# Kernel tuning notes

Measured on AMD Instinct MI355X. Metric: run time of the kernel, lower is better.

Reference implementation:

```python
import jax, jax.numpy as jnp
import numpy as np

EPS = 1e-18
MARGIN = 0.2  # hp.margin (cancels: positive/positive == 1)
BIAS = 1.0    # hp.bias


def setup_inputs() -> dict:
    key = jax.random.key(0)
    k1, k2, k3, k4 = jax.random.split(key, 4)
    B, T, D = 32, 256, 256  # T == D required by the broadcast in Ecos_sim
    return {
        "pre_VF": jax.random.normal(k1, (B, T, D), dtype=jnp.float32),
        "pre_AF": jax.random.normal(k2, (B, T, D), dtype=jnp.float32),
        "back_VF": jax.random.normal(k3, (B, T, D), dtype=jnp.float32),
        "back_AF": jax.random.normal(k4, (B, T, D), dtype=jnp.float32),
    }


def _direction_loss(V, A):
    """For each anchor i: log(1 + sum_{j != i} exp(sim(V_i, A_j))).

    sim(V_i, A_j)[t, s] = (V_i @ A_j.T)[t, s] / (||V_i||_F * colnorm(A_j)[s])
    (faithful to Ecos_sim: scalar Frobenius norm for V, per-column norm for A,
    broadcast along the last axis; positive/positive == 1 exactly, so the
    positive term and margin cancel.)
    """
    B = V.shape[0]
    # upper[i,j,t,s] = <V[i,t,:], A[j,s,:]>
    upper = jnp.einsum("itd,jsd->ijts", V, A)
    v_norm = jnp.sqrt(jnp.sum(V ** 2, axis=(1, 2)) + EPS)      # [B]
    a_norm = jnp.sqrt(jnp.sum(A ** 2, axis=1) + EPS)           # [B, D]
    sim = upper / (v_norm[:, None, None, None] * a_norm[None, :, None, :])
    e_sim = jnp.exp(sim)                                        # [B,B,T,T]
    idx = jnp.arange(B)
    down = e_sim.sum(axis=1) - e_sim[idx, idx]                  # exclude j == i
    rows = jnp.log(1.0 + down)                                  # [B,T,T]
    return rows.reshape(-1, rows.shape[-1])                     # cat along dim 0


def reference(pre_VF, pre_AF, back_VF, back_AF):
    sim_back_V = _direction_loss(back_VF, back_AF)
    sim_back_A = _direction_loss(back_AF, back_VF)
    return -(1.0 / BIAS) * (sim_back_V + sim_back_A)
```

## Files before the change

kernel.cpp:

```cpp
#include <hip/hip_runtime.h>
#include <cstdint>

#define R_TOT 8192
#define KD    256
#define SLOT  ((size_t)R_TOT * KD)
#define IVN_OFF  0
#define ICN_OFF  256
#define CSQ_OFF  (ICN_OFF + 65536)
#define MATS_OFF (CSQ_OFF + 524288)

typedef float f32x4 __attribute__((ext_vector_type(4)));
typedef int   i32x4 __attribute__((ext_vector_type(4)));
typedef int   i32x8 __attribute__((ext_vector_type(8)));

__device__ __forceinline__ void glds16(const void* g, void* l){
  __builtin_amdgcn_global_load_lds((const __attribute__((address_space(1))) uint32_t*)g,
                                   (__attribute__((address_space(3))) uint32_t*)l, 16, 0, 0);
}

__global__ void cast_ns_k(const float* __restrict__ V, const float* __restrict__ A,
                          unsigned char* __restrict__ mats, float* __restrict__ csq){
  const int tc = blockIdx.x, j = blockIdx.y, ten = blockIdx.z;
  const int tid = threadIdx.x;
  const int g    = tid & 31;
  const int tsub = tid >> 5;
  const int c    = g >> 1;
  const int half = g & 1;
  const float* X = (ten ? A : V) + (size_t)j * 65536;
  unsigned char* M = mats + (size_t)ten * SLOT + (size_t)j * 65536;
  float cs[8];
  #pragma unroll
  for (int e = 0; e < 8; ++e) cs[e] = 0.f;
  #pragma unroll
  for (int tt = 0; tt < 4; ++tt){
    const int t = tc * 32 + tt * 8 + tsub;
    const float4 p0 = *(const float4*)(X + t * 256 + g * 8);
    const float4 p1 = *(const float4*)(X + t * 256 + g * 8 + 4);
    cs[0] += p0.x * p0.x; cs[1] += p0.y * p0.y; cs[2] += p0.z * p0.z; cs[3] += p0.w * p0.w;
    cs[4] += p1.x * p1.x; cs[5] += p1.y * p1.y; cs[6] += p1.z * p1.z; cs[7] += p1.w * p1.w;
    int d0 = __builtin_amdgcn_cvt_pk_fp8_f32(p0.x, p0.y, 0, false);
    d0     = __builtin_amdgcn_cvt_pk_fp8_f32(p0.z, p0.w, d0, true);
    int d1 = __builtin_amdgcn_cvt_pk_fp8_f32(p1.x, p1.y, 0, false);
    d1     = __builtin_amdgcn_cvt_pk_fp8_f32(p1.z, p1.w, d1, true);
    int2 o; o.x = d0; o.y = d1;
    *(int2*)(M + (size_t)t * 256 + (((c ^ (t & 15)) << 4) | (half << 3))) = o;
  }
  __shared__ float red[8][256];
  #pragma unroll
  for (int e = 0; e < 8; ++e) red[tsub][g * 8 + e] = cs[e];
  __syncthreads();
  float s = 0.f;
  #pragma unroll
  for (int gg = 0; gg < 8; ++gg) s += red[gg][tid];
  csq[(size_t)((tc * 2 + ten) * 32 + j) * 256 + tid] = s;
}

__global__ void nreduce_k(const float* __restrict__ csq, float* __restrict__ ivn,
                          float* __restrict__ icn){
  const int j = blockIdx.x, ten = blockIdx.y, s = threadIdx.x;
  float c = 0.f;
  #pragma unroll
  for (int tc = 0; tc < 8; ++tc)
    c += csq[(size_t)((tc * 2 + ten) * 32 + j) * 256 + s];
  icn[ten * 8192 + j * 256 + s] = rsqrtf(c + 1e-18f);
  __shared__ float red[256];
  red[s] = c; __syncthreads();
  for (int off = 128; off > 0; off >>= 1){
    if (s < off) red[s] += red[s + off];
    __syncthreads();
  }
  if (s == 0) ivn[ten * 32 + j] = rsqrtf(red[0] + 1e-18f);
}

__global__ __launch_bounds__(256, 4) void gemm_both_k(const unsigned char* __restrict__ mats,
                                                      const float* __restrict__ ivn,
                                                      const float* __restrict__ icn,
                                                      float* __restrict__ out){
  __shared__ __align__(16) char smem[40960];
  const int tid  = threadIdx.x;
  const int lane = tid & 63;
  const int w    = tid >> 6;
  const int dir  = w >> 1;
  const int wn   = (w & 1) * 16;
  const int lm   = lane & 15;
  const int kh   = lane >> 4;
  const int s0   = blockIdx.x * 32;
  const int rb   = blockIdx.y;
  const int r0   = rb * 64;
  const int ib   = rb >> 2;

  const unsigned char* rowmat = mats + (size_t)dir * SLOT;
  const unsigned char* colmat = mats + (size_t)(1 - dir) * SLOT;
  const float sivn = ivn[dir * 32 + ib] * 1.44269504088896340736f;

  float* cscw = (float*)(smem + 32768) + w * 512;
  {
    const float* ibase = icn + (size_t)(1 - dir) * 8192 + s0 + wn;
    #pragma unroll
    for (int jx = 0; jx < 8; ++jx){
      const int j = kh * 8 + jx;
      cscw[j * 16 + lm] = sivn * ibase[j * 256 + lm];
    }
  }

  i32x8 afr[4][2];
  #pragma unroll
  for (int mi = 0; mi < 4; ++mi){
    const unsigned char* rp = rowmat + (size_t)(r0 + mi * 16 + lm) * 256;
    #pragma unroll
    for (int t = 0; t < 2; ++t){
      i32x4 lo = *(const i32x4*)(rp + ((((t << 3) | (kh << 1) | 0) ^ lm) << 4));
      i32x4 hi = *(const i32x4*)(rp + ((((t << 3) | (kh << 1) | 1) ^ lm) << 4));
      afr[mi][t] = i32x8{lo.x, lo.y, lo.z, lo.w, hi.x, hi.y, hi.z, hi.w};
    }
  }
  #pragma unroll
  for (int mi = 0; mi < 4; ++mi)
    #pragma unroll
    for (int t = 0; t < 2; ++t)
      asm volatile("" : "+v"(afr[mi][t]));

  char* wbase = smem + w * 8192;
  int ad[2][2];
  #pragma unroll
  for (int t = 0; t < 2; ++t)
    #pragma unroll
    for (int u = 0; u < 2; ++u)
      ad[t][u] = lm * 256 + ((((t << 3) | (kh << 1) | u) ^ lm) << 4);
  const int lo16 = lane * 16;

  f32x4 acc[4];
  #pragma unroll
  for (int mi = 0; mi < 4; ++mi)
    acc[mi] = f32x4{0.f, 0.f, 0.f, 0.f};

  {
    const int j0 = (ib == 0) ? 1 : 0;
    const unsigned char* src = colmat + ((size_t)j0 * 256 + s0 + wn) * 256;
    #pragma unroll
    for (int c = 0; c < 4; ++c)
      glds16(src + c * 1024 + lo16, wbase + c * 1024 + lo16);
  }
  asm volatile("s_waitcnt vmcnt(0) lgkmcnt(0)" ::: "memory");

  for (int jj = 0; jj < 31; ++jj){
    const int j = jj + (jj >= ib ? 1 : 0);

    if (jj < 30){
      const int jn = (jj + 1) + ((jj + 1) >= ib ? 1 : 0);
      const unsigned char* src = colmat + ((size_t)jn * 256 + s0 + wn) * 256;
      char* dst = wbase + (((jj + 1) & 1) << 12);
      #pragma unroll
      for (int c = 0; c < 4; ++c)
        glds16(src + c * 1024 + lo16, dst + c * 1024 + lo16);
      asm volatile("s_waitcnt vmcnt(4)" ::: "memory");
    } else {
      asm volatile("s_waitcnt vmcnt(0)" ::: "memory");
    }

    const char* rbuf = wbase + ((jj & 1) << 12);
    i32x4 lo0 = *(const i32x4*)(rbuf + ad[0][0]);
    i32x4 hi0 = *(const i32x4*)(rbuf + ad[0][1]);
    i32x4 lo1 = *(const i32x4*)(rbuf + ad[1][0]);
    i32x4 hi1 = *(const i32x4*)(rbuf + ad[1][1]);
    const float csc = cscw[j * 16 + lm];

    i32x8 b[2];
    b[0] = i32x8{lo0.x, lo0.y, lo0.z, lo0.w, hi0.x, hi0.y, hi0.z, hi0.w};
    b[1] = i32x8{lo1.x, lo1.y, lo1.z, lo1.w, hi1.x, hi1.y, hi1.z, hi1.w};

    f32x4 S[4];
    #pragma unroll
    for (int mi = 0; mi < 4; ++mi)
      S[mi] = f32x4{0.f, 0.f, 0.f, 0.f};
    #pragma unroll
    for (int t = 0; t < 2; ++t){
      S[0] = __builtin_amdgcn_mfma_scale_f32_16x16x128_f8f6f4(afr[0][t], b[t], S[0], 0, 0, 0, 127, 0, 127);
      S[1] = __builtin_amdgcn_mfma_scale_f32_16x16x128_f8f6f4(afr[1][t], b[t], S[1], 0, 0, 0, 127, 0, 127);
      S[2] = __builtin_amdgcn_mfma_scale_f32_16x16x128_f8f6f4(afr[2][t], b[t], S[2], 0, 0, 0, 127, 0, 127);
      S[3] = __builtin_amdgcn_mfma_scale_f32_16x16x128_f8f6f4(afr[3][t], b[t], S[3], 0, 0, 0, 127, 0, 127);
    }
    #pragma unroll
    for (int mi = 0; mi < 4; ++mi)
      #pragma unroll
      for (int r = 0; r < 4; ++r)
        acc[mi][r] += __builtin_amdgcn_exp2f(S[mi][r] * csc);
  }

  __syncthreads();
  float* ebuf = (float*)smem;
  #pragma unroll
  for (int mi = 0; mi < 4; ++mi){
    const int n = wn + lm;
    #pragma unroll
    for (int r = 0; r < 4; ++r){
      const int m = mi * 16 + (kh << 2) + r;
      ebuf[(dir * 64 + m) * 36 + n] = __logf(1.f + acc[mi][r]);
    }
  }
  __syncthreads();
  #pragma unroll
  for (int p = 0; p < 2; ++p){
    const int i   = tid + p * 256;
    const int row = i >> 3;
    const int c4  = i & 7;
    const f32x4 e0 = *(const f32x4*)(&ebuf[row * 36 + c4 * 4]);
    const f32x4 e1 = *(const f32x4*)(&ebuf[(64 + row) * 36 + c4 * 4]);
    f32x4 o;
    #pragma unroll
    for (int e = 0; e < 4; ++e) o[e] = -(e0[e] + e1[e]);
    *(f32x4*)(&out[(size_t)(r0 + row) * 256 + s0 + c4 * 4]) = o;
  }
}

extern "C" void kernel_launch(void* const* d_in, const int* in_sizes, int n_in,
                              void* d_out, int out_size, void* d_ws, size_t ws_size,
                              hipStream_t stream){
  const float* V = (const float*)d_in[2];
  const float* A = (const float*)d_in[3];
  float* out = (float*)d_out;
  float* ivn = (float*)((char*)d_ws + IVN_OFF);
  float* icn = (float*)((char*)d_ws + ICN_OFF);
  float* csq = (float*)((char*)d_ws + CSQ_OFF);
  unsigned char* mats = (unsigned char*)((char*)d_ws + MATS_OFF);

  cast_ns_k<<<dim3(8, 32, 2), 256, 0, stream>>>(V, A, mats, csq);
  nreduce_k<<<dim3(32, 2), 256, 0, stream>>>(csq, ivn, icn);
  gemm_both_k<<<dim3(8, 128), 256, 0, stream>>>(mats, ivn, icn, out);
}
```

Before: 118.5 us.

## Software-pipeline MFMA and exp stages with ping-pong registers in GEMM loop

The column-tile loop is restructured into a two-stage software pipeline. The MFMAs for tile x are issued while the exp2/accumulate of tile x-1 runs, using ping-pong B fragments and score registers, with sched_barrier and s_setprio to control issue order. The first global-to-LDS prefetch now starts before the A fragments are loaded. Launch bounds drop from 4 to 2 blocks per CU, which frees registers for the doubled state but may lower occupancy from the four blocks per CU that LDS allows.

```diff
diff --git a/kernel.cpp b/kernel.cpp
--- a/kernel.cpp
+++ b/kernel.cpp
@@ -72,7 +72,7 @@
   if (s == 0) ivn[ten * 32 + j] = rsqrtf(red[0] + 1e-18f);
 }
 
-__global__ __launch_bounds__(256, 4) void gemm_both_k(const unsigned char* __restrict__ mats,
+__global__ __launch_bounds__(256, 2) void gemm_both_k(const unsigned char* __restrict__ mats,
                                                       const float* __restrict__ ivn,
                                                       const float* __restrict__ icn,
                                                       float* __restrict__ out){
@@ -93,7 +93,22 @@
   const unsigned char* colmat = mats + (size_t)(1 - dir) * SLOT;
   const float sivn = ivn[dir * 32 + ib] * 1.44269504088896340736f;
 
+  char* wbase = smem + w * 8192;
   float* cscw = (float*)(smem + 32768) + w * 512;
+  const int lo16 = lane * 16;
+  const unsigned char* colbase = colmat + (size_t)(s0 + wn) * 256;
+
+  auto issue = [&](int x){
+    const int j = x + (x >= ib ? 1 : 0);
+    const unsigned char* src = colbase + (size_t)j * 65536;
+    char* dst = wbase + ((x & 1) << 12);
+    #pragma unroll
+    for (int c = 0; c < 4; ++c)
+      glds16(src + c * 1024 + lo16, dst + c * 1024 + lo16);
+  };
+
+  issue(0);
+
   {
     const float* ibase = icn + (size_t)(1 - dir) * 8192 + s0 + wn;
     #pragma unroll
@@ -120,72 +135,91 @@
     for (int t = 0; t < 2; ++t)
       asm volatile("" : "+v"(afr[mi][t]));
 
-  char* wbase = smem + w * 8192;
   int ad[2][2];
   #pragma unroll
   for (int t = 0; t < 2; ++t)
     #pragma unroll
     for (int u = 0; u < 2; ++u)
       ad[t][u] = lm * 256 + ((((t << 3) | (kh << 1) | u) ^ lm) << 4);
-  const int lo16 = lane * 16;
 
   f32x4 acc[4];
   #pragma unroll
   for (int mi = 0; mi < 4; ++mi)
     acc[mi] = f32x4{0.f, 0.f, 0.f, 0.f};
-
-  {
-    const int j0 = (ib == 0) ? 1 : 0;
-    const unsigned char* src = colmat + ((size_t)j0 * 256 + s0 + wn) * 256;
-    #pragma unroll
-    for (int c = 0; c < 4; ++c)
-      glds16(src + c * 1024 + lo16, wbase + c * 1024 + lo16);
-  }
+  const f32x4 fz = {0.f, 0.f, 0.f, 0.f};
+
+  i32x8 bA[2], bB[2];
+  f32x4 SA[4], SB[4];
+  float cscA, cscB;
+
+#define DSREAD(BX, CX, x_) do{                                                  \
+    const char* rbuf_ = wbase + (((x_) & 1) << 12);                             \
+    i32x4 lo0_ = *(const i32x4*)(rbuf_ + ad[0][0]);                             \
+    i32x4 hi0_ = *(const i32x4*)(rbuf_ + ad[0][1]);                             \
+    i32x4 lo1_ = *(const i32x4*)(rbuf_ + ad[1][0]);                             \
+    i32x4 hi1_ = *(const i32x4*)(rbuf_ + ad[1][1]);                             \
+    BX[0] = i32x8{lo0_.x, lo0_.y, lo0_.z, lo0_.w, hi0_.x, hi0_.y, hi0_.z, hi0_.w}; \
+    BX[1] = i32x8{lo1_.x, lo1_.y, lo1_.z, lo1_.w, hi1_.x, hi1_.y, hi1_.z, hi1_.w}; \
+    const int j_ = (x_) + ((x_) >= ib ? 1 : 0);                                 \
+    CX = cscw[j_ * 16 + lm];                                                    \
+  }while(0)
+
+#define MFMA8(SX, BX) do{                                                       \
+    SX[0] = __builtin_amdgcn_mfma_scale_f32_16x16x128_f8f6f4(afr[0][0], BX[0], fz,    0, 0, 0, 127, 0, 127); \
+    SX[1] = __builtin_amdgcn_mfma_scale_f32_16x16x128_f8f6f4(afr[1][0], BX[0], fz,    0, 0, 0, 127, 0, 127); \
+    SX[2] = __builtin_amdgcn_mfma_scale_f32_16x16x128_f8f6f4(afr[2][0], BX[0], fz,    0, 0, 0, 127, 0, 127); \
+    SX[3] = __builtin_amdgcn_mfma_scale_f32_16x16x128_f8f6f4(afr[3][0], BX[0], fz,    0, 0, 0, 127, 0, 127); \
+    SX[0] = __builtin_amdgcn_mfma_scale_f32_16x16x128_f8f6f4(afr[0][1], BX[1], SX[0], 0, 0, 0, 127, 0, 127); \
+    SX[1] = __builtin_amdgcn_mfma_scale_f32_16x16x128_f8f6f4(afr[1][1], BX[1], SX[1], 0, 0, 0, 127, 0, 127); \
+    SX[2] = __builtin_amdgcn_mfma_scale_f32_16x16x128_f8f6f4(afr[2][1], BX[1], SX[2], 0, 0, 0, 127, 0, 127); \
+    SX[3] = __builtin_amdgcn_mfma_scale_f32_16x16x128_f8f6f4(afr[3][1], BX[1], SX[3], 0, 0, 0, 127, 0, 127); \
+  }while(0)
+
+#define EXPACC(SY, CY) do{                                                      \
+    _Pragma("unroll")                                                           \
+    for (int mi_ = 0; mi_ < 4; ++mi_){                                          \
+      _Pragma("unroll")                                                         \
+      for (int r_ = 0; r_ < 4; ++r_)                                            \
+        acc[mi_][r_] += __builtin_amdgcn_exp2f(SY[mi_][r_] * CY);               \
+    }                                                                           \
+  }while(0)
+
+#define STEP(x_, BX, SX, CX, SY, CY, PF) do{                                    \
+    if (PF) issue((x_) + 1);                                                    \
+    if (PF) asm volatile("s_waitcnt vmcnt(4)" ::: "memory");                    \
+    else    asm volatile("s_waitcnt vmcnt(0)" ::: "memory");                    \
+    DSREAD(BX, CX, x_);                                                         \
+    asm volatile("s_waitcnt lgkmcnt(0)" ::: "memory");                          \
+    __builtin_amdgcn_sched_barrier(0);                                          \
+    __builtin_amdgcn_s_setprio(1);                                              \
+    MFMA8(SX, BX);                                                              \
+    EXPACC(SY, CY);                                                             \
+    __builtin_amdgcn_s_setprio(0);                                              \
+  }while(0)
+
   asm volatile("s_waitcnt vmcnt(0) lgkmcnt(0)" ::: "memory");
-
-  for (int jj = 0; jj < 31; ++jj){
-    const int j = jj + (jj >= ib ? 1 : 0);
-
-    if (jj < 30){
-      const int jn = (jj + 1) + ((jj + 1) >= ib ? 1 : 0);
-      const unsigned char* src = colmat + ((size_t)jn * 256 + s0 + wn) * 256;
-      char* dst = wbase + (((jj + 1) & 1) << 12);
-      #pragma unroll
-      for (int c = 0; c < 4; ++c)
-        glds16(src + c * 1024 + lo16, dst + c * 1024 + lo16);
-      asm volatile("s_waitcnt vmcnt(4)" ::: "memory");
-    } else {
-      asm volatile("s_waitcnt vmcnt(0)" ::: "memory");
-    }
-
-    const char* rbuf = wbase + ((jj & 1) << 12);
-    i32x4 lo0 = *(const i32x4*)(rbuf + ad[0][0]);
-    i32x4 hi0 = *(const i32x4*)(rbuf + ad[0][1]);
-    i32x4 lo1 = *(const i32x4*)(rbuf + ad[1][0]);
-    i32x4 hi1 = *(const i32x4*)(rbuf + ad[1][1]);
-    const float csc = cscw[j * 16 + lm];
-
-    i32x8 b[2];
-    b[0] = i32x8{lo0.x, lo0.y, lo0.z, lo0.w, hi0.x, hi0.y, hi0.z, hi0.w};
-    b[1] = i32x8{lo1.x, lo1.y, lo1.z, lo1.w, hi1.x, hi1.y, hi1.z, hi1.w};
-
-    f32x4 S[4];
-    #pragma unroll
-    for (int mi = 0; mi < 4; ++mi)
-      S[mi] = f32x4{0.f, 0.f, 0.f, 0.f};
-    #pragma unroll
-    for (int t = 0; t < 2; ++t){
-      S[0] = __builtin_amdgcn_mfma_scale_f32_16x16x128_f8f6f4(afr[0][t], b[t], S[0], 0, 0, 0, 127, 0, 127);
-      S[1] = __builtin_amdgcn_mfma_scale_f32_16x16x128_f8f6f4(afr[1][t], b[t], S[1], 0, 0, 0, 127, 0, 127);
-      S[2] = __builtin_amdgcn_mfma_scale_f32_16x16x128_f8f6f4(afr[2][t], b[t], S[2], 0, 0, 0, 127, 0, 127);
-      S[3] = __builtin_amdgcn_mfma_scale_f32_16x16x128_f8f6f4(afr[3][t], b[t], S[3], 0, 0, 0, 127, 0, 127);
-    }
-    #pragma unroll
-    for (int mi = 0; mi < 4; ++mi)
-      #pragma unroll
-      for (int r = 0; r < 4; ++r)
-        acc[mi][r] += __builtin_amdgcn_exp2f(S[mi][r] * csc);
-  }
+  __builtin_amdgcn_sched_barrier(0);
+  DSREAD(bA, cscA, 0);
+  issue(1);
+  asm volatile("s_waitcnt lgkmcnt(0)" ::: "memory");
+  __builtin_amdgcn_sched_barrier(0);
+  __builtin_amdgcn_s_setprio(1);
+  MFMA8(SA, bA);
+  __builtin_amdgcn_s_setprio(0);
+
+  #pragma unroll 1
+  for (int it = 0; it < 14; ++it){
+    STEP(2 * it + 1, bB, SB, cscB, SA, cscA, 1);
+    STEP(2 * it + 2, bA, SA, cscA, SB, cscB, 1);
+  }
+  STEP(29, bB, SB, cscB, SA, cscA, 1);
+  STEP(30, bA, SA, cscA, SB, cscB, 0);
+  EXPACC(SA, cscA);
+
+#undef STEP
+#undef EXPACC
+#undef MFMA8
+#undef DSREAD
 
   __syncthreads();
   float* ebuf = (float*)smem;
```

Result: no change. 118.1 us (-0.3%).

## Enlarge GEMM tile to 128 rows per block with 2x2 MFMA per wave

Applied to the files above, without the earlier changes.

Each block now covers 128 rows instead of 64, and each wave computes a 64x32 sub-tile (4x2 MFMA tiles) instead of 64x16. The aim is to reuse each B fragment across more A fragments and halve the number of blocks. The column tile is now loaded once per wave at 8KB per stage. LDS use doubles to 80KB and occupancy drops to 2 blocks per CU, with only 512 blocks in the grid. The accumulators are now split so that the MFMA chains across the K halves are interleaved.

```diff
diff --git a/kernel.cpp b/kernel.cpp
--- a/kernel.cpp
+++ b/kernel.cpp
@@ -72,41 +72,57 @@
   if (s == 0) ivn[ten * 32 + j] = rsqrtf(red[0] + 1e-18f);
 }
 
-__global__ __launch_bounds__(256, 4) void gemm_both_k(const unsigned char* __restrict__ mats,
+__global__ __launch_bounds__(256, 2) void gemm_both_k(const unsigned char* __restrict__ mats,
                                                       const float* __restrict__ ivn,
                                                       const float* __restrict__ icn,
                                                       float* __restrict__ out){
-  __shared__ __align__(16) char smem[40960];
+  __shared__ __align__(16) char smem[81920];
   const int tid  = threadIdx.x;
   const int lane = tid & 63;
   const int w    = tid >> 6;
   const int dir  = w >> 1;
-  const int wn   = (w & 1) * 16;
+  const int half = w & 1;
   const int lm   = lane & 15;
   const int kh   = lane >> 4;
   const int s0   = blockIdx.x * 32;
   const int rb   = blockIdx.y;
-  const int r0   = rb * 64;
-  const int ib   = rb >> 2;
+  const int r0   = rb * 128;
+  const int ib   = rb >> 1;
 
   const unsigned char* rowmat = mats + (size_t)dir * SLOT;
   const unsigned char* colmat = mats + (size_t)(1 - dir) * SLOT;
   const float sivn = ivn[dir * 32 + ib] * 1.44269504088896340736f;
 
-  float* cscw = (float*)(smem + 32768) + w * 512;
+  char* wbase = smem + w * 16384;
+  float* cscw = (float*)(smem + 65536) + w * 1024;
+  const int lo16 = lane * 16;
+  const unsigned char* colbase = colmat + (size_t)s0 * 256;
+
+  auto issue = [&](int x){
+    const int j = x + (x >= ib ? 1 : 0);
+    const unsigned char* src = colbase + (size_t)j * 65536;
+    char* dst = wbase + ((x & 1) << 13);
+    #pragma unroll
+    for (int c = 0; c < 8; ++c)
+      glds16(src + c * 1024 + lo16, dst + c * 1024 + lo16);
+  };
+
+  issue(0);
+
   {
-    const float* ibase = icn + (size_t)(1 - dir) * 8192 + s0 + wn;
-    #pragma unroll
-    for (int jx = 0; jx < 8; ++jx){
-      const int j = kh * 8 + jx;
-      cscw[j * 16 + lm] = sivn * ibase[j * 256 + lm];
+    const int col = lane & 31;
+    const float* ib2 = icn + (size_t)(1 - dir) * 8192 + s0 + col;
+    #pragma unroll
+    for (int jx = 0; jx < 16; ++jx){
+      const int j = jx * 2 + (lane >> 5);
+      cscw[j * 32 + col] = sivn * ib2[j * 256];
     }
   }
 
   i32x8 afr[4][2];
   #pragma unroll
   for (int mi = 0; mi < 4; ++mi){
-    const unsigned char* rp = rowmat + (size_t)(r0 + mi * 16 + lm) * 256;
+    const unsigned char* rp = rowmat + (size_t)(r0 + half * 64 + mi * 16 + lm) * 256;
     #pragma unroll
     for (int t = 0; t < 2; ++t){
       i32x4 lo = *(const i32x4*)(rp + ((((t << 3) | (kh << 1) | 0) ^ lm) << 4));
@@ -120,92 +136,95 @@
     for (int t = 0; t < 2; ++t)
       asm volatile("" : "+v"(afr[mi][t]));
 
-  char* wbase = smem + w * 8192;
-  int ad[2][2];
-  #pragma unroll
-  for (int t = 0; t < 2; ++t)
-    #pragma unroll
-    for (int u = 0; u < 2; ++u)
-      ad[t][u] = lm * 256 + ((((t << 3) | (kh << 1) | u) ^ lm) << 4);
-  const int lo16 = lane * 16;
-
-  f32x4 acc[4];
+  int ad[2][2][2];
+  #pragma unroll
+  for (int nj = 0; nj < 2; ++nj)
+    #pragma unroll
+    for (int t = 0; t < 2; ++t)
+      #pragma unroll
+      for (int u = 0; u < 2; ++u)
+        ad[nj][t][u] = (nj * 16 + lm) * 256 + ((((t << 3) | (kh << 1) | u) ^ lm) << 4);
+
+  f32x4 acc[4][2];
   #pragma unroll
   for (int mi = 0; mi < 4; ++mi)
-    acc[mi] = f32x4{0.f, 0.f, 0.f, 0.f};
-
-  {
-    const int j0 = (ib == 0) ? 1 : 0;
-    const unsigned char* src = colmat + ((size_t)j0 * 256 + s0 + wn) * 256;
-    #pragma unroll
-    for (int c = 0; c < 4; ++c)
-      glds16(src + c * 1024 + lo16, wbase + c * 1024 + lo16);
-  }
+    #pragma unroll
+    for (int nj = 0; nj < 2; ++nj)
+      acc[mi][nj] = f32x4{0.f, 0.f, 0.f, 0.f};
+  const f32x4 fz = {0.f, 0.f, 0.f, 0.f};
+
   asm volatile("s_waitcnt vmcnt(0) lgkmcnt(0)" ::: "memory");
 
+  #pragma unroll 1
   for (int jj = 0; jj < 31; ++jj){
     const int j = jj + (jj >= ib ? 1 : 0);
 
     if (jj < 30){
-      const int jn = (jj + 1) + ((jj + 1) >= ib ? 1 : 0);
-      const unsigned char* src = colmat + ((size_t)jn * 256 + s0 + wn) * 256;
-      char* dst = wbase + (((jj + 1) & 1) << 12);
-      #pragma unroll
-      for (int c = 0; c < 4; ++c)
-        glds16(src + c * 1024 + lo16, dst + c * 1024 + lo16);
-      asm volatile("s_waitcnt vmcnt(4)" ::: "memory");
+      issue(jj + 1);
+      asm volatile("s_waitcnt vmcnt(8)" ::: "memory");
     } else {
       asm volatile("s_waitcnt vmcnt(0)" ::: "memory");
     }
 
-    const char* rbuf = wbase + ((jj & 1) << 12);
-    i32x4 lo0 = *(const i32x4*)(rbuf + ad[0][0]);
-    i32x4 hi0 = *(const i32x4*)(rbuf + ad[0][1]);
-    i32x4 lo1 = *(const i32x4*)(rbuf + ad[1][0]);
-    i32x4 hi1 = *(const i32x4*)(rbuf + ad[1][1]);
-    const float csc = cscw[j * 16 + lm];
-
-    i32x8 b[2];
-    b[0] = i32x8{lo0.x, lo0.y, lo0.z, lo0.w, hi0.x, hi0.y, hi0.z, hi0.w};
-    b[1] = i32x8{lo1.x, lo1.y, lo1.z, lo1.w, hi1.x, hi1.y, hi1.z, hi1.w};
-
-    f32x4 S[4];
-    #pragma unroll
-    for (int mi = 0; mi < 4; ++mi)
-      S[mi] = f32x4{0.f, 0.f, 0.f, 0.f};
-    #pragma unroll
-    for (int t = 0; t < 2; ++t){
-      S[0] = __builtin_amdgcn_mfma_scale_f32_16x16x128_f8f6f4(afr[0][t], b[t], S[0], 0, 0, 0, 127, 0, 127);
-      S[1] = __builtin_amdgcn_mfma_scale_f32_16x16x128_f8f6f4(afr[1][t], b[t], S[1], 0, 0, 0, 127, 0, 127);
-      S[2] = __builtin_amdgcn_mfma_scale_f32_16x16x128_f8f6f4(afr[2][t], b[t], S[2], 0, 0, 0, 127, 0, 127);
-      S[3] = __builtin_amdgcn_mfma_scale_f32_16x16x128_f8f6f4(afr[3][t], b[t], S[3], 0, 0, 0, 127, 0, 127);
-    }
-    #pragma unroll
-    for (int mi = 0; mi < 4; ++mi)
-      #pragma unroll
-      for (int r = 0; r < 4; ++r)
-        acc[mi][r] += __builtin_amdgcn_exp2f(S[mi][r] * csc);
+    const char* rbuf = wbase + ((jj & 1) << 13);
+    i32x8 b[2][2];
+    #pragma unroll
+    for (int nj = 0; nj < 2; ++nj)
+      #pragma unroll
+      for (int t = 0; t < 2; ++t){
+        i32x4 lo = *(const i32x4*)(rbuf + ad[nj][t][0]);
+        i32x4 hi = *(const i32x4*)(rbuf + ad[nj][t][1]);
+        b[t][nj] = i32x8{lo.x, lo.y, lo.z, lo.w, hi.x, hi.y, hi.z, hi.w};
+      }
+    const float csc0 = cscw[j * 32 + lm];
+    const float csc1 = cscw[j * 32 + 16 + lm];
+
+    f32x4 S[4][2];
+    #pragma unroll
+    for (int mi = 0; mi < 4; ++mi){
+      S[mi][0] = __builtin_amdgcn_mfma_scale_f32_16x16x128_f8f6f4(afr[mi][0], b[0][0], fz, 0, 0, 0, 127, 0, 127);
+      S[mi][1] = __builtin_amdgcn_mfma_scale_f32_16x16x128_f8f6f4(afr[mi][0], b[0][1], fz, 0, 0, 0, 127, 0, 127);
+    }
+    #pragma unroll
+    for (int mi = 0; mi < 4; ++mi){
+      S[mi][0] = __builtin_amdgcn_mfma_scale_f32_16x16x128_f8f6f4(afr[mi][1], b[1][0], S[mi][0], 0, 0, 0, 127, 0, 127);
+      S[mi][1] = __builtin_amdgcn_mfma_scale_f32_16x16x128_f8f6f4(afr[mi][1], b[1][1], S[mi][1], 0, 0, 0, 127, 0, 127);
+    }
+
+    #pragma unroll
+    for (int mi = 0; mi < 4; ++mi){
+      const f32x4 t0 = S[mi][0] * csc0;
+      const f32x4 t1 = S[mi][1] * csc1;
+      f32x4 e0, e1;
+      #pragma unroll
+      for (int r = 0; r < 4; ++r){ e0[r] = __builtin_amdgcn_exp2f(t0[r]); e1[r] = __builtin_amdgcn_exp2f(t1[r]); }
+      acc[mi][0] += e0;
+      acc[mi][1] += e1;
+    }
   }
 
   __syncthreads();
   float* ebuf = (float*)smem;
   #pragma unroll
   for (int mi = 0; mi < 4; ++mi){
-    const int n = wn + lm;
-    #pragma unroll
-    for (int r = 0; r < 4; ++r){
-      const int m = mi * 16 + (kh << 2) + r;
-      ebuf[(dir * 64 + m) * 36 + n] = __logf(1.f + acc[mi][r]);
+    #pragma unroll
+    for (int nj = 0; nj < 2; ++nj){
+      const int n = nj * 16 + lm;
+      #pragma unroll
+      for (int r = 0; r < 4; ++r){
+        const int m = half * 64 + mi * 16 + (kh << 2) + r;
+        ebuf[(dir * 128 + m) * 36 + n] = __logf(1.f + acc[mi][nj][r]);
+      }
     }
   }
   __syncthreads();
   #pragma unroll
-  for (int p = 0; p < 2; ++p){
+  for (int p = 0; p < 4; ++p){
     const int i   = tid + p * 256;
     const int row = i >> 3;
     const int c4  = i & 7;
     const f32x4 e0 = *(const f32x4*)(&ebuf[row * 36 + c4 * 4]);
-    const f32x4 e1 = *(const f32x4*)(&ebuf[(64 + row) * 36 + c4 * 4]);
+    const f32x4 e1 = *(const f32x4*)(&ebuf[(128 + row) * 36 + c4 * 4]);
     f32x4 o;
     #pragma unroll
     for (int e = 0; e < 4; ++e) o[e] = -(e0[e] + e1[e]);
@@ -226,5 +245,5 @@
 
   cast_ns_k<<<dim3(8, 32, 2), 256, 0, stream>>>(V, A, mats, csq);
   nreduce_k<<<dim3(32, 2), 256, 0, stream>>>(csq, ivn, icn);
-  gemm_both_k<<<dim3(8, 128), 256, 0, stream>>>(mats, ivn, icn, out);
-}
+  gemm_both_k<<<dim3(8, 64), 256, 0, stream>>>(mats, ivn, icn, out);
+}
```

After: 120.3 us. About the same (+1.5%).
